# Performance work log

Measured on AMD Instinct MI355X. Metric: run time of the kernel, lower is better.

The kernel has to match this reference:

```python
import jax, jax.numpy as jnp
import numpy as np

H, D, K = 8, 64, 9           # new num heads, head size, conv kernel size
A = H * D                    # all_head_size = 512
HID = 2 * A                  # input hidden size = 1024
STD = 0.02


def setup_inputs() -> dict:
    key = jax.random.key(0)
    ks = jax.random.split(key, 16)
    B, S = 4, 2048
    f = jnp.float32
    inp = {
        'hidden_states': jax.random.normal(ks[0], (B, S, HID), f),
        'Wq': jax.random.normal(ks[1], (A, A), f) * STD,
        'bq': jnp.zeros((A,), f),
        'Wk': jax.random.normal(ks[2], (A, A), f) * STD,
        'bk': jnp.zeros((A,), f),
        'Wv': jax.random.normal(ks[3], (A, A), f) * STD,
        'bv': jnp.zeros((A,), f),
        'dw_w': jax.random.normal(ks[4], (A, 1, K), f) * STD,   # depthwise conv (groups=A)
        'pw_w': jax.random.normal(ks[5], (A, A, 1), f) * STD,   # pointwise 1x1 conv
        'sep_b': jnp.zeros((A, 1), f),                          # SeparableConv1D bias
        'Wck': jax.random.normal(ks[6], (H * K, A), f) * STD,   # conv_kernel_layer
        'bck': jnp.zeros((H * K,), f),
        'Wco': jax.random.normal(ks[7], (A, A), f) * STD,       # conv_out_layer
        'bco': jnp.zeros((A,), f),
    }
    return inp


def reference(hidden_states, Wq, bq, Wk, bk, Wv, bv, dw_w, pw_w, sep_b, Wck, bck, Wco, bco):
    B, S, _ = hidden_states.shape
    hs_attn = hidden_states[:, :, :A]
    hs_conv = hidden_states[:, :, A:]

    q = hs_attn @ Wq.T + bq
    k = hs_attn @ Wk.T + bk
    v = hs_attn @ Wv.T + bv

    # SeparableConv1D on (B, A, S): depthwise then pointwise, plus bias
    x = hs_conv.transpose(0, 2, 1)
    x = jax.lax.conv_general_dilated(
        x, dw_w, window_strides=(1,), padding=[(K // 2, K // 2)],
        feature_group_count=A, dimension_numbers=('NCH', 'OIH', 'NCH'))
    x = jnp.einsum('bcs,oc->bos', x, pw_w[:, :, 0]) + sep_b
    mixed_key_conv = x.transpose(0, 2, 1)            # (B,S,A)

    # per-token softmax conv kernel
    conv_attn = mixed_key_conv * hs_conv
    ckl = (conv_attn @ Wck.T + bck).reshape(B, S, H, K)
    ckl = jax.nn.softmax(ckl, axis=-1)               # softmax over kernel taps

    # dynamic-span lightweight convolution (unfold -> batched matmul)
    col = hs_conv @ Wco.T + bco                      # (B,S,A)
    pad = jnp.pad(col, ((0, 0), (K // 2, K // 2), (0, 0)))
    windows = jnp.stack([pad[:, i:i + S] for i in range(K)], axis=-1)  # (B,S,A,K)
    windows = windows.reshape(B, S, H, D, K)
    conv_out = jnp.einsum('bshdk,bshk->bshd', windows, ckl)            # (B,S,H,D)

    # standard self-attention
    qh = q.reshape(B, S, H, D).transpose(0, 2, 1, 3)
    kh = k.reshape(B, S, H, D).transpose(0, 2, 1, 3)
    vh = v.reshape(B, S, H, D).transpose(0, 2, 1, 3)
    scale = jnp.asarray(1.0 / np.sqrt(D), q.dtype)
    scores = jnp.einsum('bhqd,bhkd->bhqk', qh, kh) * scale
    probs = jax.nn.softmax(scores, axis=-1)
    ctx = jnp.einsum('bhqk,bhkd->bqhd', probs, vh)   # (B,S,H,D)

    out = jnp.concatenate([ctx, conv_out], axis=2)   # (B,S,2H,D)
    return out.reshape(B, S, HID)
```

## Files before the change

### kernel.cpp

```cpp
#include <hip/hip_runtime.h>
#include <hip/hip_bf16.h>

#define NH   8
#define HD   64
#define KW   9
#define AD   512
#define HIDD 1024
#define BB   4
#define SS   2048
#define MTOK (BB*SS)
#define WSZ  262144

typedef __attribute__((ext_vector_type(8))) short short8;
typedef __attribute__((ext_vector_type(4))) float floatx4;

__device__ __forceinline__ short f2bf(float f) {
    unsigned u = __float_as_uint(f);
    u = (u + 0x7FFFu + ((u >> 16) & 1u)) >> 16;
    return (short)u;
}
__device__ __forceinline__ float bf2f(short s) {
    return __uint_as_float(((unsigned)(unsigned short)s) << 16);
}
__device__ __forceinline__ float exp2_raw(float x) {
    return __builtin_amdgcn_exp2f(x);
}
__device__ __forceinline__ unsigned pkbf2(float a, float b) {
    unsigned au = __float_as_uint(a) + 0x8000u;
    unsigned bu = __float_as_uint(b) + 0x8000u;
    return __builtin_amdgcn_perm(bu, au, 0x07060302);
}
__device__ __forceinline__ void gl2lds16(const short* g, short* l) {
    __builtin_amdgcn_global_load_lds(
        (const __attribute__((address_space(1))) void*)g,
        (__attribute__((address_space(3))) void*)l, 16, 0, 0);
}

__global__ __launch_bounds__(256) void cvt_hs_kernel(
    const float* __restrict__ hs, short* __restrict__ hsb)
{
    int idx = blockIdx.x * 256 + threadIdx.x;
    const float* s = hs + (long)idx * 8;
    float4 a = *(const float4*)s, c = *(const float4*)(s + 4);
    short8 o;
    o[0]=f2bf(a.x); o[1]=f2bf(a.y); o[2]=f2bf(a.z); o[3]=f2bf(a.w);
    o[4]=f2bf(c.x); o[5]=f2bf(c.y); o[6]=f2bf(c.z); o[7]=f2bf(c.w);
    *(short8*)(hsb + (long)idx * 8) = o;
}

__global__ __launch_bounds__(256) void cvt_w_kernel(
    const float* __restrict__ pw, const float* __restrict__ Wco,
    const float* __restrict__ Wq, const float* __restrict__ Wk,
    const float* __restrict__ Wv, const float* __restrict__ Wck,
    const float* __restrict__ dw,
    short* __restrict__ dst, float* __restrict__ dwT)
{
    int idx = blockIdx.x * 256 + threadIdx.x;
    if (idx >= 172032) {
        int t = idx - 172032;
        if (t < AD * KW) {
            int c = t / KW, k = t - c * KW;
            dwT[k * AD + c] = dw[t];
        }
        return;
    }
    int e0 = idx * 8;
    short8 o;
    if (e0 < 5 * WSZ) {
        int w = e0 >> 18, off = e0 & (WSZ - 1);
        const float* src = (w == 0) ? pw : (w == 1) ? Wco : (w == 2) ? Wq
                         : (w == 3) ? Wk : Wv;
        float4 a = *(const float4*)(src + off), c = *(const float4*)(src + off + 4);
        o[0]=f2bf(a.x); o[1]=f2bf(a.y); o[2]=f2bf(a.z); o[3]=f2bf(a.w);
        o[4]=f2bf(c.x); o[5]=f2bf(c.y); o[6]=f2bf(c.z); o[7]=f2bf(c.w);
    } else {
        int off = e0 - 5 * WSZ;
        int row = off >> 9, col = off & 511;
        if (row < NH * KW) {
            const float* src = Wck + row * AD + col;
            float4 a = *(const float4*)src, c = *(const float4*)(src + 4);
            o[0]=f2bf(a.x); o[1]=f2bf(a.y); o[2]=f2bf(a.z); o[3]=f2bf(a.w);
            o[4]=f2bf(c.x); o[5]=f2bf(c.y); o[6]=f2bf(c.z); o[7]=f2bf(c.w);
        } else {
            for (int i = 0; i < 8; ++i) o[i] = 0;
        }
    }
    *(short8*)(dst + e0) = o;
}

__global__ __launch_bounds__(256) void dwconv_kernel(
    const short* __restrict__ hsb, const float* __restrict__ dwT,
    short* __restrict__ x1)
{
    int idx = blockIdx.x * 256 + threadIdx.x;
    int c8  = (idx & 63) * 8;
    int tok = idx >> 6;
    int s   = tok & (SS - 1);
    int b   = tok >> 11;
    const short* base = hsb + (long)(b * SS) * HIDD + AD + c8;
    float acc[8];
#pragma unroll
    for (int i = 0; i < 8; ++i) acc[i] = 0.f;
#pragma unroll
    for (int kk = 0; kk < KW; ++kk) {
        int ss2 = s + kk - KW / 2;
        if (ss2 >= 0 && ss2 < SS) {
            short8 hv = *(const short8*)(base + (long)ss2 * HIDD);
            float4 w0 = *(const float4*)(dwT + kk * AD + c8);
            float4 w1 = *(const float4*)(dwT + kk * AD + c8 + 4);
            acc[0] += w0.x * bf2f(hv[0]); acc[1] += w0.y * bf2f(hv[1]);
            acc[2] += w0.z * bf2f(hv[2]); acc[3] += w0.w * bf2f(hv[3]);
            acc[4] += w1.x * bf2f(hv[4]); acc[5] += w1.y * bf2f(hv[5]);
            acc[6] += w1.z * bf2f(hv[6]); acc[7] += w1.w * bf2f(hv[7]);
        }
    }
    short8 o;
#pragma unroll
    for (int i = 0; i < 8; ++i) o[i] = f2bf(acc[i]);
    *(short8*)(x1 + (long)tok * AD + c8) = o;
}

template<int FM, int FN, int MODE>
__global__ __launch_bounds__(256) void gemm_bf16_kernel(
    const short* __restrict__ X, int ldx, int xoff,
    const short* __restrict__ W,
    const float* __restrict__ b0p, const float* __restrict__ b1p,
    const float* __restrict__ b2p,
    const short* __restrict__ mulp, int mul_ld, int mul_off,
    void* __restrict__ Cout, short* __restrict__ vtout,
    int ldc, int N, int Kd, float oscale)
{
    constexpr int TM = 32 * FM, TN = 32 * FN;
    __shared__ __align__(16) short As[TM * 64];
    __shared__ __align__(16) short Bs[TN * 64];
    const int tid  = threadIdx.x;
    const int wv   = tid >> 6, lane = tid & 63;
    const int ln   = lane & 15, quad = lane >> 4;
    const int wm   = wv >> 1, wn = wv & 1;
    const int m0 = blockIdx.x * TM, n0 = blockIdx.y * TN;

    floatx4 acc[FM][FN];
#pragma unroll
    for (int i = 0; i < FM; ++i)
#pragma unroll
        for (int j = 0; j < FN; ++j) acc[i][j] = (floatx4){0.f, 0.f, 0.f, 0.f};

    const short* xbase = X + (long)m0 * ldx + xoff;
    const short* wbase = W + (long)n0 * Kd;

    for (int k0 = 0; k0 < Kd; k0 += 64) {
#pragma unroll
        for (int g = tid; g < TM * 8; g += 256) {
            int m = g >> 3, p = g & 7, gk = p ^ (m & 7);
            gl2lds16(xbase + (long)m * ldx + k0 + gk * 8, &As[g * 8]);
        }
#pragma unroll
        for (int g = tid; g < TN * 8; g += 256) {
            int m = g >> 3, p = g & 7, gk = p ^ (m & 7);
            gl2lds16(wbase + (long)m * Kd + k0 + gk * 8, &Bs[g * 8]);
        }
        __syncthreads();
#pragma unroll
        for (int half = 0; half < 2; ++half) {
            short8 afr[FM], bfr[FN];
#pragma unroll
            for (int i = 0; i < FM; ++i) {
                int p = (half * 4 + quad) ^ (ln & 7);
                afr[i] = *(const short8*)&As[(wm * 16 * FM + i * 16 + ln) * 64 + p * 8];
            }
#pragma unroll
            for (int j = 0; j < FN; ++j) {
                int p = (half * 4 + quad) ^ (ln & 7);
                bfr[j] = *(const short8*)&Bs[(wn * 16 * FN + j * 16 + ln) * 64 + p * 8];
            }
#pragma unroll
            for (int i = 0; i < FM; ++i)
#pragma unroll
                for (int j = 0; j < FN; ++j)
                    acc[i][j] = __builtin_amdgcn_mfma_f32_16x16x32_bf16(
                        afr[i], bfr[j], acc[i][j], 0, 0, 0);
        }
        __syncthreads();
    }

#pragma unroll
    for (int j = 0; j < FN; ++j) {
        int n = n0 + wn * 16 * FN + j * 16 + ln;
        if constexpr (MODE == 3) {
            if (n >= 1024) {
                int hh = (n - 1024) >> 6, dd = (n - 1024) & 63;
                float bv = b2p[n - 1024];
                int mblk = m0 + wm * 16 * FM;
                int bidx = mblk >> 11, sblk = mblk & (SS - 1);
                short* dst = vtout + ((long)((bidx * NH + hh) * HD + dd)) * SS + sblk;
#pragma unroll
                for (int r = 0; r < 4; ++r) {
                    unsigned lo = pkbf2(acc[0][j][r] + bv, acc[1 % FM][j][r] + bv);
                    unsigned hi = pkbf2(acc[2 % FM][j][r] + bv, acc[3 % FM][j][r] + bv);
                    *(uint2*)(dst + (quad * 4 + r) * 4) = make_uint2(lo, hi);
                }
            } else {
                float bv = (n < 512) ? b0p[n] : b1p[n - 512];
                float sc = (n < 512) ? oscale : 1.f;
#pragma unroll
                for (int i = 0; i < FM; ++i) {
#pragma unroll
                    for (int r = 0; r < 4; ++r) {
                        int m = m0 + wm * 16 * FM + i * 16 + quad * 4 + r;
                        float val = (acc[i][j][r] + bv) * sc;
                        ((short*)Cout)[(long)m * ldc + n] = f2bf(val);
                    }
                }
            }
        } else if (n < N) {
            float bv = b0p[n], sc = oscale;
#pragma unroll
            for (int i = 0; i < FM; ++i) {
#pragma unroll
                for (int r = 0; r < 4; ++r) {
                    int m = m0 + wm * 16 * FM + i * 16 + quad * 4 + r;
                    float val = (acc[i][j][r] + bv) * sc;
                    if constexpr (MODE == 2)
                        val *= bf2f(mulp[(long)m * mul_ld + mul_off + n]);
                    if constexpr (MODE == 0)
                        ((float*)Cout)[(long)m * ldc + n] = val;
                    else
                        ((short*)Cout)[(long)m * ldc + n] = f2bf(val);
                }
            }
        }
    }
}

__global__ __launch_bounds__(256) void convout_kernel(
    const short* __restrict__ col, const float* __restrict__ ckl,
    float* __restrict__ out)
{
    int idx = blockIdx.x * 256 + threadIdx.x;
    int d4  = (idx & 127) * 4;
    int tok = idx >> 7;
    int s   = tok & (SS - 1);
    int b   = tok >> 11;
    int h   = d4 >> 6;
    const float* lg = ckl + (long)tok * (NH * KW) + h * KW;
    float wv[KW];
    float mx = -1e30f;
#pragma unroll
    for (int i = 0; i < KW; ++i) { wv[i] = lg[i]; mx = fmaxf(mx, wv[i]); }
    float sum = 0.f;
#pragma unroll
    for (int i = 0; i < KW; ++i) { wv[i] = __expf(wv[i] - mx); sum += wv[i]; }
    float inv = 1.f / sum;
    float a0 = 0.f, a1 = 0.f, a2 = 0.f, a3 = 0.f;
    const short* cbase = col + (long)(b * SS) * AD + d4;
#pragma unroll
    for (int kk = 0; kk < KW; ++kk) {
        int ss2 = s + kk - KW / 2;
        if (ss2 >= 0 && ss2 < SS) {
            uint2 cv = *(const uint2*)(cbase + (long)ss2 * AD);
            float w = wv[kk];
            a0 += w * bf2f((short)(cv.x & 0xFFFF));
            a1 += w * bf2f((short)(cv.x >> 16));
            a2 += w * bf2f((short)(cv.y & 0xFFFF));
            a3 += w * bf2f((short)(cv.y >> 16));
        }
    }
    *(float4*)&out[(long)tok * HIDD + AD + d4] =
        make_float4(a0 * inv, a1 * inv, a2 * inv, a3 * inv);
}

__global__ __launch_bounds__(256) void flash_mfma_kernel(
    const short* __restrict__ qkv, const short* __restrict__ vT,
    float* __restrict__ out)
{
    const int qt = blockIdx.x, h = blockIdx.y, b = blockIdx.z;
    const int tid  = threadIdx.x;
    const int w    = tid >> 6;
    const int lane = tid & 63;
    const int ln   = lane & 15;
    const int quad = lane >> 4;

    __shared__ __align__(16) short Kb[64 * 64];
    __shared__ __align__(16) short Vt[64 * 64];
    __shared__ __align__(16) short Ps[4][16 * 72];

    const int  q0 = qt * 64;
    const long rowbase = (long)b * SS;

    short8 qa[2];
    {
        const short* qrow = qkv + (rowbase + q0 + w * 16 + ln) * 1536 + h * HD;
        qa[0] = *(const short8*)(qrow + quad * 8);
        qa[1] = *(const short8*)(qrow + 32 + quad * 8);
    }

    floatx4 acc[4];
    float l_i[4];
#pragma unroll
    for (int r = 0; r < 4; ++r) {
        l_i[r] = 0.f;
        acc[r] = (floatx4){0.f, 0.f, 0.f, 0.f};
    }

    const int m1 = tid >> 3,  gk1 = (tid & 7) ^ (m1 & 7);
    const int g2 = 256 + tid;
    const int m2 = g2 >> 3,   gk2 = (g2 & 7) ^ (m2 & 7);
    const short* kbase  = qkv + 512 + rowbase * 1536 + h * HD;
    const short* vtbase = vT + ((long)(b * NH + h) * HD) * SS;
    const short* sk0 = kbase  + (long)m1 * 1536 + gk1 * 8;
    const short* sk1 = kbase  + (long)m2 * 1536 + gk2 * 8;
    const short* sv0 = vtbase + (long)m1 * SS   + gk1 * 8;
    const short* sv1 = vtbase + (long)m2 * SS   + gk2 * 8;
    short* const dk0 = &Kb[tid * 8];
    short* const dk1 = &Kb[g2 * 8];
    short* const dv0 = &Vt[tid * 8];
    short* const dv1 = &Vt[g2 * 8];

#define STAGE_K() do { gl2lds16(sk0, dk0); gl2lds16(sk1, dk1); \
                       sk0 += 64 * 1536; sk1 += 64 * 1536; } while (0)
#define STAGE_V() do { gl2lds16(sv0, dv0); gl2lds16(sv1, dv1); \
                       sv0 += 64; sv1 += 64; } while (0)

    auto qkt_phase = [&]() {
        floatx4 S[4];
#pragma unroll
        for (int st = 0; st < 4; ++st) {
            int p0i = quad ^ (ln & 7), p1i = (4 + quad) ^ (ln & 7);
            short8 b0 = *(const short8*)&Kb[(st * 16 + ln) * 64 + p0i * 8];
            short8 b1 = *(const short8*)&Kb[(st * 16 + ln) * 64 + p1i * 8];
            floatx4 z = (floatx4){0.f, 0.f, 0.f, 0.f};
            z = __builtin_amdgcn_mfma_f32_16x16x32_bf16(qa[0], b0, z, 0, 0, 0);
            S[st] = __builtin_amdgcn_mfma_f32_16x16x32_bf16(qa[1], b1, z, 0, 0, 0);
        }
#pragma unroll
        for (int r = 0; r < 4; ++r) {
            float p0 = exp2_raw(S[0][r]);
            float p1 = exp2_raw(S[1][r]);
            float p2 = exp2_raw(S[2][r]);
            float p3 = exp2_raw(S[3][r]);
            l_i[r] += (p0 + p1) + (p2 + p3);
            unsigned lo = pkbf2(p0, p1);
            unsigned hi = pkbf2(p2, p3);
            *(uint2*)&Ps[w][(quad * 4 + r) * 72 + ln * 4] = make_uint2(lo, hi);
        }
    };

    auto pv_phase = [&]() {
        short8 pa0 = *(const short8*)&Ps[w][ln * 72 + quad * 8];
        short8 pa1 = *(const short8*)&Ps[w][ln * 72 + 32 + quad * 8];
#pragma unroll
        for (int st = 0; st < 4; ++st) {
            int p0i = quad ^ (ln & 7), p1i = (4 + quad) ^ (ln & 7);
            short8 vb0 = *(const short8*)&Vt[(st * 16 + ln) * 64 + p0i * 8];
            short8 vb1 = *(const short8*)&Vt[(st * 16 + ln) * 64 + p1i * 8];
            acc[st] = __builtin_amdgcn_mfma_f32_16x16x32_bf16(pa0, vb0, acc[st], 0, 0, 0);
            acc[st] = __builtin_amdgcn_mfma_f32_16x16x32_bf16(pa1, vb1, acc[st], 0, 0, 0);
        }
    };

    STAGE_K();
    STAGE_V();
    asm volatile("s_waitcnt vmcnt(0)" ::: "memory");
    __builtin_amdgcn_s_barrier();
    asm volatile("" ::: "memory");

    const int NT = SS / 64;
    for (int kt = 0; kt < NT - 1; ++kt) {
        qkt_phase();
        __builtin_amdgcn_s_barrier();
        asm volatile("" ::: "memory");
        STAGE_K();
        asm volatile("s_waitcnt vmcnt(2)" ::: "memory");
        __builtin_amdgcn_s_barrier();
        asm volatile("" ::: "memory");
        pv_phase();
        __builtin_amdgcn_s_barrier();
        asm volatile("" ::: "memory");
        STAGE_V();
        asm volatile("s_waitcnt vmcnt(2)" ::: "memory");
        __builtin_amdgcn_s_barrier();
        asm volatile("" ::: "memory");
    }
    qkt_phase();
    asm volatile("s_waitcnt vmcnt(0)" ::: "memory");
    __builtin_amdgcn_s_barrier();
    asm volatile("" ::: "memory");
    pv_phase();

#undef STAGE_K
#undef STAGE_V

#pragma unroll
    for (int r = 0; r < 4; ++r) {
#pragma unroll
        for (int off = 1; off < 16; off <<= 1)
            l_i[r] += __shfl_xor(l_i[r], off);
    }

#pragma unroll
    for (int r = 0; r < 4; ++r) {
        float inv = 1.f / l_i[r];
        float* orow = out + (rowbase + q0 + w * 16 + quad * 4 + r) * HIDD + h * HD;
#pragma unroll
        for (int st = 0; st < 4; ++st)
            orow[st * 16 + ln] = acc[st][r] * inv;
    }
}

extern "C" void kernel_launch(void* const* d_in, const int* in_sizes, int n_in,
                              void* d_out, int out_size, void* d_ws, size_t ws_size,
                              hipStream_t stream)
{
    const float* hs   = (const float*)d_in[0];
    const float* Wq   = (const float*)d_in[1];
    const float* bq   = (const float*)d_in[2];
    const float* Wk   = (const float*)d_in[3];
    const float* bk   = (const float*)d_in[4];
    const float* Wv   = (const float*)d_in[5];
    const float* bv   = (const float*)d_in[6];
    const float* dw   = (const float*)d_in[7];
    const float* pw   = (const float*)d_in[8];
    const float* sepb = (const float*)d_in[9];
    const float* Wck  = (const float*)d_in[10];
    const float* bck  = (const float*)d_in[11];
    const float* Wco  = (const float*)d_in[12];
    const float* bco  = (const float*)d_in[13];
    float* out = (float*)d_out;

    short* hsb  = (short*)d_ws;
    short* x1c  = hsb + (long)MTOK * HIDD;
    short* qkvb = x1c + (long)MTOK * AD;
    short* vTb  = qkvb + (long)MTOK * 1536;
    float* ckl  = (float*)(vTb + (long)MTOK * AD);
    short* wb   = (short*)(ckl + (long)MTOK * (NH * KW));
    short* pw_b   = wb;
    short* Wco_b  = wb + 1L * WSZ;
    short* Wqkv_b = wb + 2L * WSZ;
    short* Wck_b  = wb + 5L * WSZ;
    float* dwT    = (float*)(Wck_b + 128L * AD);
    short* cab    = qkvb;

    const float QSCALE = 0.18033688011112042f;

    cvt_hs_kernel<<<MTOK * HIDD / 2048, 256, 0, stream>>>(hs, hsb);
    cvt_w_kernel<<<690, 256, 0, stream>>>(
        pw, Wco, Wq, Wk, Wv, Wck, dw, wb, dwT);
    dwconv_kernel<<<MTOK * AD / 2048, 256, 0, stream>>>(hsb, dwT, x1c);
    gemm_bf16_kernel<2, 2, 2><<<dim3(MTOK / 64, AD / 64), 256, 0, stream>>>(
        x1c, AD, 0, pw_b, sepb, nullptr, nullptr, hsb, HIDD, AD,
        cab, nullptr, AD, AD, AD, 1.f);
    gemm_bf16_kernel<2, 2, 0><<<dim3(MTOK / 64, 2), 256, 0, stream>>>(
        cab, AD, 0, Wck_b, bck, nullptr, nullptr, nullptr, 0, 0,
        ckl, nullptr, NH * KW, NH * KW, AD, 1.f);
    gemm_bf16_kernel<2, 2, 1><<<dim3(MTOK / 64, AD / 64), 256, 0, stream>>>(
        hsb, HIDD, AD, Wco_b, bco, nullptr, nullptr, nullptr, 0, 0,
        x1c, nullptr, AD, AD, AD, 1.f);
    convout_kernel<<<MTOK * AD / 1024, 256, 0, stream>>>(x1c, ckl, out);
    gemm_bf16_kernel<4, 4, 3><<<dim3(MTOK / 128, 1536 / 128), 256, 0, stream>>>(
        hsb, HIDD, 0, Wqkv_b, bq, bk, bv, nullptr, 0, 0,
        qkvb, vTb, 1536, 1536, AD, QSCALE);
    flash_mfma_kernel<<<dim3(SS / 64, NH, BB), 256, 0, stream>>>(qkvb, vTb, out);

    (void)in_sizes; (void)n_in; (void)out_size; (void)ws_size;
}
```

Baseline: 223.3 us.

## Switch flash attention to 32x32x16 MFMA with in-register P via permlane swap

The attention kernel now has each wave handle 32 query rows using 32x32x16 bf16 MFMA instructions, with 128 queries per block. S is computed as K·Q^T so that the exponentiated probabilities can be packed into PV operands in registers with v_permlane32_swap, removing the LDS round trip for P. Each staged K/V tile is therefore reused by twice as many queries, but the grid has half as many blocks and each thread holds more accumulator registers. The V-transpose store in the QKV GEMM epilogue is also rewritten to loop over FM fragments instead of indexing across them.

```diff
diff --git a/kernel.cpp b/kernel.cpp
--- a/kernel.cpp
+++ b/kernel.cpp
@@ -13,6 +13,7 @@
 
 typedef __attribute__((ext_vector_type(8))) short short8;
 typedef __attribute__((ext_vector_type(4))) float floatx4;
+typedef __attribute__((ext_vector_type(16))) float floatx16;
 
 __device__ __forceinline__ short f2bf(float f) {
     unsigned u = __float_as_uint(f);
@@ -194,10 +195,10 @@
                 int bidx = mblk >> 11, sblk = mblk & (SS - 1);
                 short* dst = vtout + ((long)((bidx * NH + hh) * HD + dd)) * SS + sblk;
 #pragma unroll
-                for (int r = 0; r < 4; ++r) {
-                    unsigned lo = pkbf2(acc[0][j][r] + bv, acc[1 % FM][j][r] + bv);
-                    unsigned hi = pkbf2(acc[2 % FM][j][r] + bv, acc[3 % FM][j][r] + bv);
-                    *(uint2*)(dst + (quad * 4 + r) * 4) = make_uint2(lo, hi);
+                for (int i = 0; i < FM; ++i) {
+                    unsigned lo = pkbf2(acc[i][j][0] + bv, acc[i][j][1] + bv);
+                    unsigned hi = pkbf2(acc[i][j][2] + bv, acc[i][j][3] + bv);
+                    *(uint2*)(dst + i * 16 + quad * 4) = make_uint2(lo, hi);
                 }
             } else {
                 float bv = (n < 512) ? b0p[n] : b1p[n - 512];
@@ -277,30 +278,28 @@
     const int tid  = threadIdx.x;
     const int w    = tid >> 6;
     const int lane = tid & 63;
-    const int ln   = lane & 15;
-    const int quad = lane >> 4;
+    const int l5   = lane & 31;
+    const int hh   = lane >> 5;
 
     __shared__ __align__(16) short Kb[64 * 64];
     __shared__ __align__(16) short Vt[64 * 64];
-    __shared__ __align__(16) short Ps[4][16 * 72];
-
-    const int  q0 = qt * 64;
+    __shared__ float ls[4][32];
+
+    const int  q0 = qt * 128 + w * 32;
     const long rowbase = (long)b * SS;
 
-    short8 qa[2];
+    short8 qf[4];
     {
-        const short* qrow = qkv + (rowbase + q0 + w * 16 + ln) * 1536 + h * HD;
-        qa[0] = *(const short8*)(qrow + quad * 8);
-        qa[1] = *(const short8*)(qrow + 32 + quad * 8);
-    }
-
-    floatx4 acc[4];
-    float l_i[4];
-#pragma unroll
-    for (int r = 0; r < 4; ++r) {
-        l_i[r] = 0.f;
-        acc[r] = (floatx4){0.f, 0.f, 0.f, 0.f};
-    }
+        const short* qrow = qkv + (rowbase + q0 + l5) * 1536 + h * HD;
+#pragma unroll
+        for (int i = 0; i < 4; ++i)
+            qf[i] = *(const short8*)(qrow + i * 16 + hh * 8);
+    }
+
+    floatx16 acc0, acc1;
+#pragma unroll
+    for (int r = 0; r < 16; ++r) { acc0[r] = 0.f; acc1[r] = 0.f; }
+    float l_i = 0.f;
 
     const int m1 = tid >> 3,  gk1 = (tid & 7) ^ (m1 & 7);
     const int g2 = 256 + tid;
@@ -321,40 +320,54 @@
 #define STAGE_V() do { gl2lds16(sv0, dv0); gl2lds16(sv1, dv1); \
                        sv0 += 64; sv1 += 64; } while (0)
 
-    auto qkt_phase = [&]() {
-        floatx4 S[4];
-#pragma unroll
-        for (int st = 0; st < 4; ++st) {
-            int p0i = quad ^ (ln & 7), p1i = (4 + quad) ^ (ln & 7);
-            short8 b0 = *(const short8*)&Kb[(st * 16 + ln) * 64 + p0i * 8];
-            short8 b1 = *(const short8*)&Kb[(st * 16 + ln) * 64 + p1i * 8];
-            floatx4 z = (floatx4){0.f, 0.f, 0.f, 0.f};
-            z = __builtin_amdgcn_mfma_f32_16x16x32_bf16(qa[0], b0, z, 0, 0, 0);
-            S[st] = __builtin_amdgcn_mfma_f32_16x16x32_bf16(qa[1], b1, z, 0, 0, 0);
-        }
-#pragma unroll
-        for (int r = 0; r < 4; ++r) {
-            float p0 = exp2_raw(S[0][r]);
-            float p1 = exp2_raw(S[1][r]);
-            float p2 = exp2_raw(S[2][r]);
-            float p3 = exp2_raw(S[3][r]);
-            l_i[r] += (p0 + p1) + (p2 + p3);
-            unsigned lo = pkbf2(p0, p1);
-            unsigned hi = pkbf2(p2, p3);
-            *(uint2*)&Ps[w][(quad * 4 + r) * 72 + ln * 4] = make_uint2(lo, hi);
+    auto qkt_pack = [&](short8* pf) {
+        floatx16 S0, S1;
+#pragma unroll
+        for (int r = 0; r < 16; ++r) { S0[r] = 0.f; S1[r] = 0.f; }
+#pragma unroll
+        for (int i = 0; i < 4; ++i) {
+            int p = (2 * i + hh) ^ (l5 & 7);
+            short8 k0 = *(const short8*)&Kb[l5 * 64 + p * 8];
+            short8 k1 = *(const short8*)&Kb[(32 + l5) * 64 + p * 8];
+            S0 = __builtin_amdgcn_mfma_f32_32x32x16_bf16(k0, qf[i], S0, 0, 0, 0);
+            S1 = __builtin_amdgcn_mfma_f32_32x32x16_bf16(k1, qf[i], S1, 0, 0, 0);
+        }
+        float pe0[16], pe1[16];
+#pragma unroll
+        for (int r = 0; r < 16; ++r) {
+            pe0[r] = exp2_raw(S0[r]);
+            pe1[r] = exp2_raw(S1[r]);
+        }
+        float s = 0.f;
+#pragma unroll
+        for (int r = 0; r < 16; ++r) s += pe0[r] + pe1[r];
+        l_i += s;
+#pragma unroll
+        for (int t = 0; t < 2; ++t) {
+            const float* pe = t ? pe1 : pe0;
+#pragma unroll
+            for (int u = 0; u < 2; ++u) {
+                unsigned a0 = pkbf2(pe[8 * u + 0], pe[8 * u + 1]);
+                unsigned a1 = pkbf2(pe[8 * u + 2], pe[8 * u + 3]);
+                unsigned b0 = pkbf2(pe[8 * u + 4], pe[8 * u + 5]);
+                unsigned b1 = pkbf2(pe[8 * u + 6], pe[8 * u + 7]);
+                asm("v_permlane32_swap_b32 %0, %1" : "+v"(a0), "+v"(b0));
+                asm("v_permlane32_swap_b32 %0, %1" : "+v"(a1), "+v"(b1));
+                union { uint4 u4; short8 s8; } cv;
+                cv.u4 = make_uint4(a0, a1, b0, b1);
+                pf[t * 2 + u] = cv.s8;
+            }
         }
     };
 
-    auto pv_phase = [&]() {
-        short8 pa0 = *(const short8*)&Ps[w][ln * 72 + quad * 8];
-        short8 pa1 = *(const short8*)&Ps[w][ln * 72 + 32 + quad * 8];
-#pragma unroll
-        for (int st = 0; st < 4; ++st) {
-            int p0i = quad ^ (ln & 7), p1i = (4 + quad) ^ (ln & 7);
-            short8 vb0 = *(const short8*)&Vt[(st * 16 + ln) * 64 + p0i * 8];
-            short8 vb1 = *(const short8*)&Vt[(st * 16 + ln) * 64 + p1i * 8];
-            acc[st] = __builtin_amdgcn_mfma_f32_16x16x32_bf16(pa0, vb0, acc[st], 0, 0, 0);
-            acc[st] = __builtin_amdgcn_mfma_f32_16x16x32_bf16(pa1, vb1, acc[st], 0, 0, 0);
+    auto pv_phase = [&](const short8* pf) {
+#pragma unroll
+        for (int s = 0; s < 4; ++s) {
+            int p = (2 * s + hh) ^ (l5 & 7);
+            short8 v0 = *(const short8*)&Vt[l5 * 64 + p * 8];
+            short8 v1 = *(const short8*)&Vt[(32 + l5) * 64 + p * 8];
+            acc0 = __builtin_amdgcn_mfma_f32_32x32x16_bf16(pf[s], v0, acc0, 0, 0, 0);
+            acc1 = __builtin_amdgcn_mfma_f32_32x32x16_bf16(pf[s], v1, acc1, 0, 0, 0);
         }
     };
 
@@ -365,15 +378,16 @@
     asm volatile("" ::: "memory");
 
     const int NT = SS / 64;
+    short8 pf[4];
     for (int kt = 0; kt < NT - 1; ++kt) {
-        qkt_phase();
+        qkt_pack(pf);
         __builtin_amdgcn_s_barrier();
         asm volatile("" ::: "memory");
         STAGE_K();
         asm volatile("s_waitcnt vmcnt(2)" ::: "memory");
         __builtin_amdgcn_s_barrier();
         asm volatile("" ::: "memory");
-        pv_phase();
+        pv_phase(pf);
         __builtin_amdgcn_s_barrier();
         asm volatile("" ::: "memory");
         STAGE_V();
@@ -381,29 +395,30 @@
         __builtin_amdgcn_s_barrier();
         asm volatile("" ::: "memory");
     }
-    qkt_phase();
+    qkt_pack(pf);
     asm volatile("s_waitcnt vmcnt(0)" ::: "memory");
     __builtin_amdgcn_s_barrier();
     asm volatile("" ::: "memory");
-    pv_phase();
+    pv_phase(pf);
 
 #undef STAGE_K
 #undef STAGE_V
 
-#pragma unroll
-    for (int r = 0; r < 4; ++r) {
-#pragma unroll
-        for (int off = 1; off < 16; off <<= 1)
-            l_i[r] += __shfl_xor(l_i[r], off);
-    }
-
-#pragma unroll
-    for (int r = 0; r < 4; ++r) {
-        float inv = 1.f / l_i[r];
-        float* orow = out + (rowbase + q0 + w * 16 + quad * 4 + r) * HIDD + h * HD;
-#pragma unroll
-        for (int st = 0; st < 4; ++st)
-            orow[st * 16 + ln] = acc[st][r] * inv;
+    l_i += __shfl_xor(l_i, 32);
+    ls[w][l5] = 1.f / l_i;
+    float4 lv[4];
+#pragma unroll
+    for (int g = 0; g < 4; ++g)
+        lv[g] = *(const float4*)&ls[w][8 * g + 4 * hh];
+
+#pragma unroll
+    for (int r = 0; r < 16; ++r) {
+        int g = r >> 2, j = r & 3;
+        int qr = j + 8 * g + 4 * hh;
+        float iv = lv[g][j];
+        float* orow = out + (rowbase + q0 + qr) * HIDD + h * HD;
+        orow[l5]      = acc0[r] * iv;
+        orow[32 + l5] = acc1[r] * iv;
     }
 }
 
@@ -459,7 +474,7 @@
     gemm_bf16_kernel<4, 4, 3><<<dim3(MTOK / 128, 1536 / 128), 256, 0, stream>>>(
         hsb, HIDD, 0, Wqkv_b, bq, bk, bv, nullptr, 0, 0,
         qkvb, vTb, 1536, 1536, AD, QSCALE);
-    flash_mfma_kernel<<<dim3(SS / 64, NH, BB), 256, 0, stream>>>(qkvb, vTb, out);
+    flash_mfma_kernel<<<dim3(SS / 128, NH, BB), 256, 0, stream>>>(qkvb, vTb, out);
 
     (void)in_sizes; (void)n_in; (void)out_size; (void)ws_size;
 }
```

Result: slower. 232.9 us (+4.3%).
